# Performance work log

Hardware: AMD Instinct MI355X
Metric: run time of the kernel (lower is better)

The kernel has to match this reference:

```python
import jax, jax.numpy as jnp
import numpy as np

# ---------- p4m group (8 elements: index = mirror*4 + rotation) ----------
def _elem(i):
    return (i // 4, i % 4)

def _mul(g1, g2):
    a1, b1 = g1; a2, b2 = g2
    return ((a1 + a2) % 2, ((b1 if a2 == 0 else -b1) + b2) % 4)

def _inv(g):
    a, b = g
    return (a, (-b if a == 0 else b) % 4)

def _idx(g):
    return g[0] * 4 + g[1]

# PERM[g, h] = index of g^{-1} * h  (static table)
PERM = np.array([[_idx(_mul(_inv(_elem(g)), _elem(h))) for h in range(8)] for g in range(8)])

def _spatial_transform(w, g):
    # act on last two (spatial) axes of a kernel by group element g = (mirror, rot)
    a, b = _elem(g)
    if a:
        w = jnp.flip(w, axis=-1)
    return jnp.rot90(w, k=b, axes=(-2, -1))

def _transform_kernel(w, g):
    # w: [C_out, C_in, 8, k, k] -> kernel for output group element g
    return _spatial_transform(w[:, :, PERM[g]], g)

# ---------- BatchNorm3d (eval mode, per-channel stats) ----------
BN_EPS = 2e-5

def _bn(x, gamma, beta, mean, var):
    # x: [B, C, 8, H, W]
    inv = gamma / jnp.sqrt(var + BN_EPS)
    return x * inv[None, :, None, None, None] + (beta - mean * inv)[None, :, None, None, None]

# ---------- fChannelAttentionGG (CBAM-style, equivariant over h axis) ----------
def _channel_att(x, w1, w2):
    # x: [B, C, 8, H, W]; w1: [mid, C*8]; w2: [C*8, mid]
    avg = x.mean(axis=(-2, -1))   # [B, C, 8]
    mx = x.max(axis=(-2, -1))     # [B, C, 8]
    B, C, _ = avg.shape
    def mlp(v, g):
        v = v[:, :, PERM[g]].reshape(B, C * 8)
        return jax.nn.relu(v @ w1.T) @ w2.T   # [B, C*8]
    atts = [jax.nn.sigmoid(mlp(avg, g) + mlp(mx, g)).reshape(B, C, 8) for g in range(8)]
    return jnp.stack(atts, axis=1)            # [B, 8(out), C, 8(in)]

# ---------- fSpatialAttentionGG (7x7 conv over avg/max channel maps) ----------
SP_K = 7
SP_PAD = SP_K // 2

def _spatial_att(x, w):
    # x: [B, C, 8, H, W]; w: [2, 8, 7, 7]
    f = jnp.stack([x.mean(axis=1), x.max(axis=1)], axis=1)     # [B, 2, 8, H, W]
    B, _, _, H, W = f.shape
    f2 = f.reshape(B, 16, H, W)
    atts = []
    for g in range(8):
        wg = _spatial_transform(w[:, PERM[g]], g).reshape(1, 16, SP_K, SP_K)
        o = jax.lax.conv_general_dilated(f2, wg, (1, 1), [(SP_PAD, SP_PAD)] * 2)
        atts.append(jax.nn.sigmoid(o[:, 0]))                   # [B, H, W]
    return jnp.stack(atts, axis=1)                             # [B, 8(out), H, W]

# ---------- fAttConvGG ----------
def _att_conv_gg(x, w, ca_w1, ca_w2, sa_w, padding):
    # x: [B, C_in, 8, H, W]; w: [C_out, C_in, 8, k, k]
    ac = _channel_att(x, ca_w1, ca_w2)     # [B, 8, C_in, 8]
    sp = _spatial_att(x, sa_w)             # [B, 8, H, W]
    B, Cin, _, H, W = x.shape
    Cout, _, _, k, _ = w.shape
    outs = []
    for g in range(8):
        xg = x * ac[:, g][:, :, :, None, None] * sp[:, g][:, None, None, :, :]
        xg = xg.reshape(B, Cin * 8, H, W)
        wg = _transform_kernel(w, g).reshape(Cout, Cin * 8, k, k)
        outs.append(jax.lax.conv_general_dilated(xg, wg, (1, 1), [(padding, padding)] * 2))
    return jnp.stack(outs, axis=2)         # [B, C_out, 8, H, W]


def setup_inputs() -> dict:
    key = jax.random.key(0)
    ks = jax.random.split(key, 16)
    B, C, H, W = 8, 64, 64, 64
    mid = C // (C // 2)  # = 2, per ratio = in_channels // 2
    s_conv = 1.0 / np.sqrt(C * 8 * 9)
    inp = {
        'x': jax.random.normal(ks[0], (B, C, 8, H, W), jnp.float32),
        'bn1_gamma': jnp.ones((C,), jnp.float32),
        'bn1_beta': jnp.zeros((C,), jnp.float32),
        'bn1_mean': 0.1 * jax.random.normal(ks[1], (C,), jnp.float32),
        'bn1_var': jax.random.uniform(ks[2], (C,), jnp.float32) + 0.5,
        'w1': s_conv * jax.random.normal(ks[3], (C, C, 8, 3, 3), jnp.float32),
        'ca1_w1': jax.random.normal(ks[4], (mid, C * 8), jnp.float32) / np.sqrt(C * 8),
        'ca1_w2': jax.random.normal(ks[5], (C * 8, mid), jnp.float32) / np.sqrt(mid),
        'sa1_w': jax.random.normal(ks[6], (2, 8, SP_K, SP_K), jnp.float32) / np.sqrt(16 * SP_K * SP_K),
        'bn2_gamma': jnp.ones((C,), jnp.float32),
        'bn2_beta': jnp.zeros((C,), jnp.float32),
        'bn2_mean': 0.1 * jax.random.normal(ks[7], (C,), jnp.float32),
        'bn2_var': jax.random.uniform(ks[8], (C,), jnp.float32) + 0.5,
        'w2': s_conv * jax.random.normal(ks[9], (C, C, 8, 3, 3), jnp.float32),
        'ca2_w1': jax.random.normal(ks[10], (mid, C * 8), jnp.float32) / np.sqrt(C * 8),
        'ca2_w2': jax.random.normal(ks[11], (C * 8, mid), jnp.float32) / np.sqrt(mid),
        'sa2_w': jax.random.normal(ks[12], (2, 8, SP_K, SP_K), jnp.float32) / np.sqrt(16 * SP_K * SP_K),
    }
    return inp


def reference(x, bn1_gamma, bn1_beta, bn1_mean, bn1_var, w1, ca1_w1, ca1_w2, sa1_w,
              bn2_gamma, bn2_beta, bn2_mean, bn2_var, w2, ca2_w1, ca2_w2, sa2_w):
    h = _att_conv_gg(jax.nn.relu(_bn(x, bn1_gamma, bn1_beta, bn1_mean, bn1_var)),
                     w1, ca1_w1, ca1_w2, sa1_w, padding=1)
    h = _att_conv_gg(jax.nn.relu(_bn(h, bn2_gamma, bn2_beta, bn2_mean, bn2_var)),
                     w2, ca2_w1, ca2_w2, sa2_w, padding=1)
    return x + h  # fiber_map = identity, stride = 1 (no pooling)
```

## Files before the change

kernel.cpp:

```cpp
#include <hip/hip_runtime.h>
#include <stdint.h>

#define B_    8
#define CCH   64
#define HW_   4096
#define C512  512

typedef __attribute__((ext_vector_type(8))) short short8v;
typedef __attribute__((ext_vector_type(4))) float f32x4;
typedef __attribute__((ext_vector_type(4))) unsigned short ushort4v;

__device__ __constant__ int PERM[8][8] = {
  {0,1,2,3,4,5,6,7},
  {3,0,1,2,5,6,7,4},
  {2,3,0,1,6,7,4,5},
  {1,2,3,0,7,4,5,6},
  {4,5,6,7,0,1,2,3},
  {5,6,7,4,3,0,1,2},
  {6,7,4,5,2,3,0,1},
  {7,4,5,6,1,2,3,0},
};

__device__ inline float bf2f(unsigned int u){
  union { unsigned int i; float f; } v; v.i = u << 16; return v.f;
}
__device__ inline unsigned short f2bf(float f){
  union { float f; unsigned int i; } v; v.f = f;
  return (unsigned short)((v.i + 0x7FFFu + ((v.i >> 16) & 1u)) >> 16);
}
__device__ inline unsigned int scale2(unsigned int packed, float a0, float a1, float f){
  float v0 = bf2f(packed & 0xffffu) * a0 * f;
  float v1 = bf2f(packed >> 16)     * a1 * f;
  unsigned int i0 = __float_as_uint(v0), i1 = __float_as_uint(v1);
  return ((i0 + 0x8000u) >> 16) | ((i1 + 0x8000u) & 0xffff0000u);
}
__device__ inline float sigmoidf_(float x){ return 1.f / (1.f + __expf(-x)); }

__device__ __forceinline__ void gload_lds16(const unsigned short* g, unsigned short* l){
  __builtin_amdgcn_global_load_lds(
      (const __attribute__((address_space(1))) unsigned int*)(g),
      (__attribute__((address_space(3))) unsigned int*)(l), 16, 0, 0);
}

template<int BF>
__device__ __forceinline__ void bnrelu_body(
    const float* __restrict__ xf, const unsigned short* __restrict__ xb,
    const float* __restrict__ gamma, const float* __restrict__ beta,
    const float* __restrict__ mean,  const float* __restrict__ var,
    unsigned short* __restrict__ yT,
    float* __restrict__ csum, unsigned int* __restrict__ cmax,
    float* __restrict__ f2, int bid){
  __shared__ float lds[64 * 66];
  int b  = bid >> 9;
  int r  = bid & 511;
  int ct = r >> 6, pt = r & 63;
  int c0 = ct * 64, p0 = pt * 64;
  int t  = threadIdx.x;
  int cc = t >> 2, q = t & 3;
  int c512 = c0 + cc;
  int ch = c512 >> 3;
  float inv = gamma[ch] * rsqrtf(var[ch] + 2e-5f);
  float sh  = beta[ch] - mean[ch] * inv;
  float s_ = 0.f, m_ = 0.f;
#pragma unroll
  for (int i = 0; i < 4; ++i){
    float r0, r1, r2, r3;
    if (BF){
      const unsigned short* src = xb + ((size_t)(b * C512 + c512)) * HW_ + p0;
      ushort4v u = *(const ushort4v*)(src + i * 16 + q * 4);
      r0 = bf2f(u[0]); r1 = bf2f(u[1]); r2 = bf2f(u[2]); r3 = bf2f(u[3]);
    } else {
      const float* src = xf + ((size_t)(b * C512 + c512)) * HW_ + p0;
      float4 v = *(const float4*)(src + i * 16 + q * 4);
      r0 = v.x; r1 = v.y; r2 = v.z; r3 = v.w;
    }
    float a0 = fmaxf(r0 * inv + sh, 0.f);
    float a1 = fmaxf(r1 * inv + sh, 0.f);
    float a2 = fmaxf(r2 * inv + sh, 0.f);
    float a3 = fmaxf(r3 * inv + sh, 0.f);
    int pp = i * 16 + q * 4;
    lds[(pp + 0) * 66 + cc] = a0;
    lds[(pp + 1) * 66 + cc] = a1;
    lds[(pp + 2) * 66 + cc] = a2;
    lds[(pp + 3) * 66 + cc] = a3;
    s_ += (a0 + a1) + (a2 + a3);
    m_ = fmaxf(m_, fmaxf(fmaxf(a0, a1), fmaxf(a2, a3)));
  }
  s_ += __shfl_down(s_, 2); s_ += __shfl_down(s_, 1);
  m_ = fmaxf(m_, __shfl_down(m_, 2)); m_ = fmaxf(m_, __shfl_down(m_, 1));
  if (q == 0){
    atomicAdd(&csum[b * C512 + c512], s_);
    atomicMax(&cmax[b * C512 + c512], __float_as_uint(m_));
  }
  __syncthreads();
  int cc4 = (t & 15) * 4, g0 = t >> 4;
  unsigned short* dst = yT + ((size_t)(b * HW_ + p0)) * C512 + c0 + cc4;
#pragma unroll
  for (int i = 0; i < 4; ++i){
    int pp = i * 16 + g0;
    float2 v0 = *(const float2*)&lds[pp * 66 + cc4];
    float2 v1 = *(const float2*)&lds[pp * 66 + cc4 + 2];
    ushort4v o;
    o[0] = f2bf(v0.x); o[1] = f2bf(v0.y); o[2] = f2bf(v1.x); o[3] = f2bf(v1.y);
    *(ushort4v*)(dst + (size_t)pp * C512) = o;
  }
#pragma unroll
  for (int k = 0; k < 2; ++k){
    int task = t + k * 256;
    int px = task >> 3, s = task & 7;
    const float* row = &lds[px * 66 + s];
    float sm = row[0], mx = row[0];
#pragma unroll
    for (int j = 1; j < 8; ++j){ float v = row[j * 8]; sm += v; mx = fmaxf(mx, v); }
    atomicAdd(&f2[((size_t)(b * 2 + 0) * 8 + s) * 4096 + p0 + px], sm);
    atomicMax((unsigned int*)&f2[((size_t)(b * 2 + 1) * 8 + s) * 4096 + p0 + px],
              __float_as_uint(mx));
  }
}

template<int BF>
__global__ void k_bnrelu_tr(const float* __restrict__ xf, const unsigned short* __restrict__ xb,
                            const float* __restrict__ gamma, const float* __restrict__ beta,
                            const float* __restrict__ mean,  const float* __restrict__ var,
                            unsigned short* __restrict__ yT,
                            float* __restrict__ csum, unsigned int* __restrict__ cmax,
                            float* __restrict__ f2){
  bnrelu_body<BF>(xf, xb, gamma, beta, mean, var, yT, csum, cmax, f2, blockIdx.x);
}

__device__ __forceinline__ void cw_body(const float* __restrict__ w,
                                        unsigned short* __restrict__ wt, int e){
  int j  = e & 7;
  int co = (e >> 3) & 63;
  int kl = (e >> 9) & 3;
  int r  = e >> 11;
  int tap = r % 9; int r2 = r / 9;
  int kc = r2 & 15; int g = r2 >> 4;
  int c512 = kc * 32 + kl * 8 + j;
  int ci = c512 >> 3, s = c512 & 7;
  int ty = tap / 3, tx = tap % 3;
  int a = g >> 2, bb = g & 3;
  int sy, sx;
  if      (bb == 0){ sy = ty;     sx = tx;     }
  else if (bb == 1){ sy = tx;     sx = 2 - ty; }
  else if (bb == 2){ sy = 2 - ty; sx = 2 - tx; }
  else             { sy = 2 - tx; sx = ty;     }
  if (a) sx = 2 - sx;
  int ps = PERM[g][s];
  wt[e] = f2bf(w[((size_t)(co * 64 + ci) * 8 + ps) * 9 + sy * 3 + sx]);
}

__global__ void k_cw(const float* __restrict__ w, unsigned short* __restrict__ wt,
                     unsigned int* __restrict__ zbuf, float* __restrict__ f2){
  int e = blockIdx.x * 256 + threadIdx.x;
  if (e < 16384) zbuf[e] = 0u;
  if (e < 524288) f2[e] = 0.f;
  if (e >= 8 * 16 * 9 * 4 * 64 * 8) return;
  cw_body(w, wt, e);
}

__global__ void k_cwbn(const float* __restrict__ w, unsigned short* __restrict__ wt,
                       const unsigned short* __restrict__ h1b,
                       const float* __restrict__ gamma, const float* __restrict__ beta,
                       const float* __restrict__ mean,  const float* __restrict__ var,
                       unsigned short* __restrict__ yT,
                       float* __restrict__ csum, unsigned int* __restrict__ cmax,
                       float* __restrict__ f2){
  int bid = blockIdx.x;
  if (bid < 9216){
    int e = bid * 256 + threadIdx.x;
    if (e < 8 * 16 * 9 * 4 * 64 * 8) cw_body(w, wt, e);
    return;
  }
  bnrelu_body<1>(nullptr, h1b, gamma, beta, mean, var, yT, csum, cmax, f2, bid - 9216);
}

__global__ void k_att(const float* __restrict__ f2, const float* __restrict__ saw,
                      float* __restrict__ sp,
                      const float* __restrict__ csum, const unsigned int* __restrict__ cmax,
                      const float* __restrict__ w1, const float* __restrict__ w2,
                      float* __restrict__ ac){
  __shared__ __align__(16) float shm[16260];
  int bid = blockIdx.x;
  int t = threadIdx.x;
  if (bid < 64){
    float* vA = shm;
    float* vM = shm + 512;
    float* wred = shm + 1024;
    float* rr = shm + 1040;
    int b = bid >> 3, g = bid & 7;
    for (int j = t; j < 512; j += 256){
      int c = j >> 3, h = j & 7;
      int srcj = (c << 3) + PERM[g][h];
      vA[j] = csum[b * 512 + srcj] * (1.f / 4096.f);
      vM[j] = __uint_as_float(cmax[b * 512 + srcj]);
    }
    __syncthreads();
    float pa0 = 0, pa1 = 0, pm0 = 0, pm1 = 0;
    for (int j = t; j < 512; j += 256){
      float wa = w1[j], wb = w1[512 + j];
      pa0 += vA[j] * wa; pa1 += vA[j] * wb;
      pm0 += vM[j] * wa; pm1 += vM[j] * wb;
    }
#pragma unroll
    for (int off = 32; off >= 1; off >>= 1){
      pa0 += __shfl_down(pa0, off); pa1 += __shfl_down(pa1, off);
      pm0 += __shfl_down(pm0, off); pm1 += __shfl_down(pm1, off);
    }
    int wv = t >> 6, ln = t & 63;
    if (ln == 0){ wred[wv*4+0] = pa0; wred[wv*4+1] = pa1; wred[wv*4+2] = pm0; wred[wv*4+3] = pm1; }
    __syncthreads();
    if (t == 0){
      float hA0 = wred[0] + wred[4] + wred[8]  + wred[12];
      float hA1 = wred[1] + wred[5] + wred[9]  + wred[13];
      float hM0 = wred[2] + wred[6] + wred[10] + wred[14];
      float hM1 = wred[3] + wred[7] + wred[11] + wred[15];
      rr[0] = fmaxf(hA0, 0.f) + fmaxf(hM0, 0.f);
      rr[1] = fmaxf(hA1, 0.f) + fmaxf(hM1, 0.f);
    }
    __syncthreads();
    float r0 = rr[0], r1 = rr[1];
    for (int j = t; j < 512; j += 256){
      float z = r0 * w2[j * 2] + r1 * w2[j * 2 + 1];
      ac[(size_t)(b * 8 + g) * 512 + j] = sigmoidf_(z);
    }
    return;
  }
  float* slab = shm;
  float* wspl = shm + 8960;
  float* part = shm + 15232;
  int sb = bid - 64;
  int b = sb >> 5, strip = sb & 31;
  int R0 = strip * 2;
  for (int i = t; i < 6272; i += 256){
    int g = i & 7; int r = i >> 3;
    int kx = r % 7; int r2 = r / 7;
    int ky = r2 % 7; int tc = r2 / 7;
    int m = tc >> 3, s = tc & 7;
    int a = g >> 2, bb = g & 3;
    int sy, sx;
    if      (bb == 0){ sy = ky;     sx = kx;     }
    else if (bb == 1){ sy = kx;     sx = 6 - ky; }
    else if (bb == 2){ sy = 6 - ky; sx = 6 - kx; }
    else             { sy = 6 - kx; sx = ky;     }
    if (a) sx = 6 - sx;
    int ps = PERM[g][s];
    float wv_ = saw[((m * 8 + ps) * 7 + sy) * 7 + sx];
    wspl[i] = (m == 0) ? wv_ * 0.015625f : wv_;
  }
  for (int i = t; i < 8960; i += 256){
    int tc = i / 560; int rem = i - tc * 560;
    int rr = rem / 70; int cc = rem - rr * 70;
    int gr = R0 + rr - 3, gc = cc - 3;
    float v = 0.f;
    if ((unsigned)gr < 64u && (unsigned)gc < 64u)
      v = f2[((size_t)(b * 16 + tc)) * 4096 + gr * 64 + gc];
    slab[i] = v;
  }
  __syncthreads();
  int tcH = t >> 7, p = t & 127;
  int r = p >> 6, x = p & 63;
  float acc[8] = {0,0,0,0,0,0,0,0};
  for (int tc = tcH * 8; tc < tcH * 8 + 8; ++tc){
    const float* sl = &slab[tc * 560 + r * 70 + x];
    for (int ky = 0; ky < 7; ++ky){
#pragma unroll
      for (int kx = 0; kx < 7; ++kx){
        float v = sl[ky * 70 + kx];
        const float* w8 = &wspl[((tc * 7 + ky) * 7 + kx) * 8];
#pragma unroll
        for (int g = 0; g < 8; ++g) acc[g] += v * w8[g];
      }
    }
  }
  if (tcH == 1){
#pragma unroll
    for (int g = 0; g < 8; ++g) part[p * 8 + g] = acc[g];
  }
  __syncthreads();
  if (tcH == 0){
    int px = strip * 128 + p;
#pragma unroll
    for (int g = 0; g < 8; ++g){
      float z = acc[g] + part[p * 8 + g];
      sp[((size_t)(b * 8 + g)) * 4096 + px] = sigmoidf_(z);
    }
  }
}

template<int RES>
__global__ __launch_bounds__(256, 2)
void k_conv(const unsigned short* __restrict__ yT, const unsigned short* __restrict__ wt,
            const float* __restrict__ ac, const float* __restrict__ sp,
            const float* __restrict__ resid, float* __restrict__ outF,
            unsigned short* __restrict__ outB, float* __restrict__ f2z){
  __shared__ __align__(16) unsigned short xl[4 * 396 * 8];
  __shared__ __align__(16) unsigned short wl[9 * 4 * 64 * 8];
  __shared__ float acs[512];
  int bid0 = blockIdx.x;
  int t = threadIdx.x;
  if (RES == 0){
    *(float2*)&f2z[(size_t)(bid0 * 256 + t) * 2] = make_float2(0.f, 0.f);
  }
  int bid = (bid0 & 7) * 128 + (bid0 >> 3);
  int b = bid >> 7, g = (bid >> 4) & 7, tile = bid & 15;
  int r0 = tile * 4;
  int wv = t >> 6, ln = t & 63;
  int lrow = ln & 15, lkg = ln >> 4;
  int cg = t & 3;

  const unsigned short* ybase = yT + ((size_t)b * HW_) * C512;
  const unsigned short* wbase = wt + ((size_t)g) * 16 * 9 * 2048;
  const float* spb = sp + ((size_t)(b * 8 + g)) * 4096;

  unsigned int goff[7];
  float        fsc[7];
  int          xwb[7];
  uint4        xr[7];
#pragma unroll
  for (int it = 0; it < 7; ++it){
    int task = t + it * 256;
    bool act = (it < 6) || (t < 48);
    int hp = task >> 2;
    int hr = hp / 66, hc = hp - hr * 66;
    int gh = r0 + hr - 1, gw = hc - 1;
    bool inb = act && ((unsigned)gh < 64u) && ((unsigned)gw < 64u);
    goff[it] = inb ? (unsigned)((gh * 64 + gw) * C512 + cg * 8) : 0u;
    fsc[it]  = inb ? spb[gh * 64 + gw] : 0.f;
    xwb[it]  = (cg * 396 + hp) * 8;
  }

#pragma unroll
  for (int it = 0; it < 9; ++it){
    int task = t + it * 256;
    gload_lds16(wbase + (size_t)task * 8, &wl[(size_t)task * 8]);
  }
#pragma unroll
  for (int it = 0; it < 7; ++it)
    xr[it] = *(const uint4*)(ybase + goff[it]);
  for (int j = t; j < 512; j += 256) acs[j] = ac[(size_t)(b * 8 + g) * 512 + j];

  f32x4 acc[4][4];
#pragma unroll
  for (int mi = 0; mi < 4; ++mi)
#pragma unroll
    for (int ni = 0; ni < 4; ++ni)
      acc[mi][ni] = (f32x4){0.f, 0.f, 0.f, 0.f};
  __syncthreads();

  {
    float4 a8lo = *(const float4*)&acs[cg * 8];
    float4 a8hi = *(const float4*)&acs[cg * 8 + 4];
#pragma unroll
    for (int it = 0; it < 7; ++it){
      if (it < 6 || t < 48){
        float f = fsc[it];
        uint4 u = xr[it]; uint4 o;
        o.x = scale2(u.x, a8lo.x, a8lo.y, f);
        o.y = scale2(u.y, a8lo.z, a8lo.w, f);
        o.z = scale2(u.z, a8hi.x, a8hi.y, f);
        o.w = scale2(u.w, a8hi.z, a8hi.w, f);
        *(uint4*)&xl[xwb[it]] = o;
      }
    }
  }

  for (int kc = 0; kc < 16; ++kc){
    __syncthreads();
    if (kc < 15){
#pragma unroll
      for (int it = 0; it < 7; ++it)
        xr[it] = *(const uint4*)(ybase + goff[it] + (kc + 1) * 32);
    }
    __builtin_amdgcn_sched_barrier(0);
    __builtin_amdgcn_s_setprio(1);
#pragma unroll
    for (int tap = 0; tap < 9; ++tap){
      const int ty = tap / 3, tx = tap % 3;
      short8v a[4], bv[4];
#pragma unroll
      for (int mi = 0; mi < 4; ++mi)
        a[mi] = *(const short8v*)&wl[(size_t)((tap * 4 + lkg) * 64 + mi * 16 + lrow) * 8];
#pragma unroll
      for (int ni = 0; ni < 4; ++ni){
        int hp = (wv + ty) * 66 + ni * 16 + lrow + tx;
        bv[ni] = *(const short8v*)&xl[(size_t)(lkg * 396 + hp) * 8];
      }
#pragma unroll
      for (int mi = 0; mi < 4; ++mi)
#pragma unroll
        for (int ni = 0; ni < 4; ++ni)
          acc[mi][ni] = __builtin_amdgcn_mfma_f32_16x16x32_bf16(a[mi], bv[ni], acc[mi][ni], 0, 0, 0);
    }
    __builtin_amdgcn_s_setprio(0);
    __syncthreads();
    if (kc < 15){
      const unsigned short* wkc = wbase + (size_t)(kc + 1) * 9 * 2048;
#pragma unroll
      for (int it = 0; it < 9; ++it){
        int task = t + it * 256;
        gload_lds16(wkc + (size_t)task * 8, &wl[(size_t)task * 8]);
      }
      int cb = (kc + 1) * 32;
      float4 a8lo = *(const float4*)&acs[cb + cg * 8];
      float4 a8hi = *(const float4*)&acs[cb + cg * 8 + 4];
#pragma unroll
      for (int it = 0; it < 7; ++it){
        if (it < 6 || t < 48){
          float f = fsc[it];
          uint4 u = xr[it]; uint4 o;
          o.x = scale2(u.x, a8lo.x, a8lo.y, f);
          o.y = scale2(u.y, a8lo.z, a8lo.w, f);
          o.z = scale2(u.z, a8hi.x, a8hi.y, f);
          o.w = scale2(u.w, a8hi.z, a8hi.w, f);
          *(uint4*)&xl[xwb[it]] = o;
        }
      }
    }
  }

#pragma unroll
  for (int mi = 0; mi < 4; ++mi){
#pragma unroll
    for (int ni = 0; ni < 4; ++ni){
      int n = wv * 64 + ni * 16 + lrow;
      int rr_ = n >> 6, ww = n & 63;
      int gh = r0 + rr_;
#pragma unroll
      for (int q = 0; q < 4; ++q){
        int co = mi * 16 + (ln >> 4) * 4 + q;
        size_t oidx = ((size_t)(b * 64 + co) * 8 + g) * 4096 + gh * 64 + ww;
        if (RES){
          outF[oidx] = acc[mi][ni][q] + resid[oidx];
        } else {
          outB[oidx] = f2bf(acc[mi][ni][q]);
        }
      }
    }
  }
}

extern "C" void kernel_launch(void* const* d_in, const int* in_sizes, int n_in,
                              void* d_out, int out_size, void* d_ws, size_t ws_size,
                              hipStream_t stream){
  const size_t off_yT  = 0;
  const size_t off_wt  = off_yT  + 33554432;
  const size_t off_f2  = off_wt  + 4718592;
  const size_t off_sp  = off_f2  + 2097152;
  const size_t off_cs0 = off_sp  + 1048576;
  const size_t off_cm0 = off_cs0 + 16384;
  const size_t off_cs1 = off_cm0 + 16384;
  const size_t off_cm1 = off_cs1 + 16384;
  const size_t off_ac  = off_cm1 + 16384;
  const size_t total   = off_ac  + 1048576;
  if (ws_size < total) return;

  char* ws = (char*)d_ws;
  unsigned short* yT  = (unsigned short*)(ws + off_yT);
  unsigned short* wtb = (unsigned short*)(ws + off_wt);
  float* f2    = (float*)(ws + off_f2);
  float* spb   = (float*)(ws + off_sp);
  float* csum0 = (float*)(ws + off_cs0);
  unsigned int* cmax0 = (unsigned int*)(ws + off_cm0);
  float* csum1 = (float*)(ws + off_cs1);
  unsigned int* cmax1 = (unsigned int*)(ws + off_cm1);
  float* acb   = (float*)(ws + off_ac);

  const float* x = (const float*)d_in[0];
  unsigned short* h1b = (unsigned short*)((char*)d_out + 33554432);

  k_cw<<<9216, 256, 0, stream>>>((const float*)d_in[5], wtb, (unsigned int*)csum0, f2);
  k_bnrelu_tr<0><<<4096, 256, 0, stream>>>(x, nullptr,
      (const float*)d_in[1], (const float*)d_in[2], (const float*)d_in[3], (const float*)d_in[4],
      yT, csum0, cmax0, f2);
  k_att<<<320, 256, 0, stream>>>(f2, (const float*)d_in[8], spb, csum0, cmax0,
      (const float*)d_in[6], (const float*)d_in[7], acb);
  k_conv<0><<<1024, 256, 0, stream>>>(yT, wtb, acb, spb, nullptr, nullptr, h1b, f2);

  k_cwbn<<<13312, 256, 0, stream>>>((const float*)d_in[13], wtb, h1b,
      (const float*)d_in[9], (const float*)d_in[10], (const float*)d_in[11], (const float*)d_in[12],
      yT, csum1, cmax1, f2);
  k_att<<<320, 256, 0, stream>>>(f2, (const float*)d_in[16], spb, csum1, cmax1,
      (const float*)d_in[14], (const float*)d_in[15], acb);
  k_conv<1><<<1024, 256, 0, stream>>>(yT, wtb, acb, spb, x, (float*)d_out, nullptr, nullptr);
}
```

Before: 403.9 us.

## Load conv weights directly from global into registers with tap double-buffering

Removes the LDS staging buffer for conv weights: each lane now reads its A-fragment straight from global memory, double-buffered across taps so the next tap's weights load while the current tap's MFMAs run. This drops the global_load_lds traffic, about 36KB of LDS per block, and the LDS reads of weights, which may allow more resident blocks. In exchange every wave fetches weights redundantly from global or L2, and MFMAs now wait on global load latency. The sched_barrier is also removed, giving the compiler freedom to interleave.

```diff
diff --git a/kernel.cpp b/kernel.cpp
--- a/kernel.cpp
+++ b/kernel.cpp
@@ -35,12 +35,6 @@
   return ((i0 + 0x8000u) >> 16) | ((i1 + 0x8000u) & 0xffff0000u);
 }
 __device__ inline float sigmoidf_(float x){ return 1.f / (1.f + __expf(-x)); }
-
-__device__ __forceinline__ void gload_lds16(const unsigned short* g, unsigned short* l){
-  __builtin_amdgcn_global_load_lds(
-      (const __attribute__((address_space(1))) unsigned int*)(g),
-      (__attribute__((address_space(3))) unsigned int*)(l), 16, 0, 0);
-}
 
 template<int BF>
 __device__ __forceinline__ void bnrelu_body(
@@ -288,6 +282,28 @@
   }
 }
 
+#define WLOADTAP(TAP, AV)                                                               \
+  {                                                                                     \
+    _Pragma("unroll")                                                                   \
+    for (int mi = 0; mi < 4; ++mi)                                                      \
+      AV[mi] = *(const short8v*)(wkc + (TAP) * 2048 + mi * 128);                        \
+  }
+#define MFMATAP(TAP, AV)                                                                \
+  {                                                                                     \
+    const int ty_ = (TAP) / 3, tx_ = (TAP) % 3;                                         \
+    short8v bv[4];                                                                      \
+    _Pragma("unroll")                                                                   \
+    for (int ni = 0; ni < 4; ++ni){                                                     \
+      int hp = (wv + ty_) * 66 + ni * 16 + lrow + tx_;                                  \
+      bv[ni] = *(const short8v*)&xl[(size_t)(lkg * 396 + hp) * 8];                      \
+    }                                                                                   \
+    _Pragma("unroll")                                                                   \
+    for (int mi = 0; mi < 4; ++mi)                                                      \
+      _Pragma("unroll")                                                                 \
+      for (int ni = 0; ni < 4; ++ni)                                                    \
+        acc[mi][ni] = __builtin_amdgcn_mfma_f32_16x16x32_bf16(AV[mi], bv[ni], acc[mi][ni], 0, 0, 0); \
+  }
+
 template<int RES>
 __global__ __launch_bounds__(256, 2)
 void k_conv(const unsigned short* __restrict__ yT, const unsigned short* __restrict__ wt,
@@ -295,7 +311,6 @@
             const float* __restrict__ resid, float* __restrict__ outF,
             unsigned short* __restrict__ outB, float* __restrict__ f2z){
   __shared__ __align__(16) unsigned short xl[4 * 396 * 8];
-  __shared__ __align__(16) unsigned short wl[9 * 4 * 64 * 8];
   __shared__ float acs[512];
   int bid0 = blockIdx.x;
   int t = threadIdx.x;
@@ -311,6 +326,7 @@
 
   const unsigned short* ybase = yT + ((size_t)b * HW_) * C512;
   const unsigned short* wbase = wt + ((size_t)g) * 16 * 9 * 2048;
+  const unsigned short* wlane = wbase + (size_t)(lkg * 64 + lrow) * 8;
   const float* spb = sp + ((size_t)(b * 8 + g)) * 4096;
 
   unsigned int goff[7];
@@ -331,11 +347,6 @@
   }
 
 #pragma unroll
-  for (int it = 0; it < 9; ++it){
-    int task = t + it * 256;
-    gload_lds16(wbase + (size_t)task * 8, &wl[(size_t)task * 8]);
-  }
-#pragma unroll
   for (int it = 0; it < 7; ++it)
     xr[it] = *(const uint4*)(ybase + goff[it]);
   for (int j = t; j < 512; j += 256) acs[j] = ac[(size_t)(b * 8 + g) * 512 + j];
@@ -367,40 +378,37 @@
 
   for (int kc = 0; kc < 16; ++kc){
     __syncthreads();
+    const unsigned short* wkc = wlane + (size_t)kc * 18432;
     if (kc < 15){
 #pragma unroll
       for (int it = 0; it < 7; ++it)
         xr[it] = *(const uint4*)(ybase + goff[it] + (kc + 1) * 32);
     }
-    __builtin_amdgcn_sched_barrier(0);
     __builtin_amdgcn_s_setprio(1);
-#pragma unroll
-    for (int tap = 0; tap < 9; ++tap){
-      const int ty = tap / 3, tx = tap % 3;
-      short8v a[4], bv[4];
-#pragma unroll
-      for (int mi = 0; mi < 4; ++mi)
-        a[mi] = *(const short8v*)&wl[(size_t)((tap * 4 + lkg) * 64 + mi * 16 + lrow) * 8];
-#pragma unroll
-      for (int ni = 0; ni < 4; ++ni){
-        int hp = (wv + ty) * 66 + ni * 16 + lrow + tx;
-        bv[ni] = *(const short8v*)&xl[(size_t)(lkg * 396 + hp) * 8];
-      }
-#pragma unroll
-      for (int mi = 0; mi < 4; ++mi)
-#pragma unroll
-        for (int ni = 0; ni < 4; ++ni)
-          acc[mi][ni] = __builtin_amdgcn_mfma_f32_16x16x32_bf16(a[mi], bv[ni], acc[mi][ni], 0, 0, 0);
+    {
+      short8v aA[4], aB[4];
+      WLOADTAP(0, aA)
+      WLOADTAP(1, aB)
+      MFMATAP(0, aA)
+      WLOADTAP(2, aA)
+      MFMATAP(1, aB)
+      WLOADTAP(3, aB)
+      MFMATAP(2, aA)
+      WLOADTAP(4, aA)
+      MFMATAP(3, aB)
+      WLOADTAP(5, aB)
+      MFMATAP(4, aA)
+      WLOADTAP(6, aA)
+      MFMATAP(5, aB)
+      WLOADTAP(7, aB)
+      MFMATAP(6, aA)
+      WLOADTAP(8, aA)
+      MFMATAP(7, aB)
+      MFMATAP(8, aA)
     }
     __builtin_amdgcn_s_setprio(0);
     __syncthreads();
     if (kc < 15){
-      const unsigned short* wkc = wbase + (size_t)(kc + 1) * 9 * 2048;
-#pragma unroll
-      for (int it = 0; it < 9; ++it){
-        int task = t + it * 256;
-        gload_lds16(wkc + (size_t)task * 8, &wl[(size_t)task * 8]);
-      }
       int cb = (kc + 1) * 32;
       float4 a8lo = *(const float4*)&acs[cb + cg * 8];
       float4 a8hi = *(const float4*)&acs[cb + cg * 8 + 4];
```

Result: slower. 792.5 us (+96.2%).
